# Kernel optimization log

Measured on AMD Instinct MI355X. Metric: run time of the kernel, lower is better.

## Reference

```python
import jax, jax.numpy as jnp
import numpy as np

B, L, D = 8, 2048, 1024

def setup_inputs() -> dict:
    key = jax.random.key(0)
    ks = jax.random.split(key, 12)
    s = 1.0 / np.sqrt(D)
    return {
        "q": jax.random.normal(ks[0], (B, L, D), jnp.float32),
        "k": jax.random.normal(ks[1], (B, L, D), jnp.float32),
        "v": jax.random.normal(ks[2], (B, L, D), jnp.float32),
        "mask": jnp.ones((B, L), jnp.float32),
        # Linear params stored as [in, out] so y = x @ W + b
        "Wq": jax.random.normal(ks[3], (D, D), jnp.float32) * s,
        "bq": jnp.zeros((D,), jnp.float32),
        "Wk": jax.random.normal(ks[4], (D, D), jnp.float32) * s,
        "bk": jnp.zeros((D,), jnp.float32),
        "Wv": jax.random.normal(ks[5], (D, D), jnp.float32) * s,
        "bv": jnp.zeros((D,), jnp.float32),
        "Wg": jax.random.normal(ks[6], (2 * D, D), jnp.float32) * (1.0 / np.sqrt(2 * D)),
        "bg": jnp.zeros((D,), jnp.float32),
    }

def reference(q, k, v, mask, Wq, bq, Wk, bk, Wv, bv, Wg, bg):
    q0 = q
    qp = q @ Wq + bq          # [B, Lq, D]
    kp = k @ Wk + bk          # [B, Lk, D]
    vp = v @ Wv + bv          # [B, Lk, D]
    scale = 1.0 / jnp.sqrt(jnp.asarray(qp.shape[-1], qp.dtype))
    w = jnp.einsum('bqd,bkd->bqk', qp, kp) * scale
    w = jax.nn.softmax(w, axis=-1)          # dim=2 == last axis for 3-D
    x = jnp.einsum('bqk,bkd->bqd', w, vp)
    gate = jnp.concatenate((qp, x), axis=-1) @ Wg + bg
    x = x * mask[..., None]
    x = x * jax.nn.sigmoid(gate)
    return x + q0  # add=True
```

## Files before the change

### kernel.cpp

```cpp
#include <hip/hip_runtime.h>

typedef unsigned int u32;
typedef unsigned short u16;
using v4f    = __attribute__((ext_vector_type(4))) float;
using short8 = __attribute__((ext_vector_type(8))) short;

#define GAS __attribute__((address_space(1)))
#define LAS __attribute__((address_space(3)))

__device__ __forceinline__ u16 f2bf(float f){
  u32 u = __builtin_bit_cast(u32, f);
  u32 r = (u + 0x7fffu + ((u >> 16) & 1u)) >> 16;
  return (u16)r;
}
__device__ __forceinline__ float bf2f(u16 h){
  u32 u = ((u32)h) << 16;
  return __builtin_bit_cast(float, u);
}

__device__ __forceinline__ void gld_lds16(const void* g, void* l){
  __builtin_amdgcn_global_load_lds((const GAS u32*)g, (LAS u32*)l, 16, 0, 0);
}

__global__ __launch_bounds__(256) void cvt_f32_bf16(
    const float* __restrict__ in, u16* __restrict__ out)
{
  const size_t i = ((size_t)blockIdx.x * 256 + threadIdx.x) * 8;
  v4f lo = *(const v4f*)(in + i);
  v4f hi = *(const v4f*)(in + i + 4);
  u32 p0 = (u32)f2bf(lo.x) | ((u32)f2bf(lo.y) << 16);
  u32 p1 = (u32)f2bf(lo.z) | ((u32)f2bf(lo.w) << 16);
  u32 p2 = (u32)f2bf(hi.x) | ((u32)f2bf(hi.y) << 16);
  u32 p3 = (u32)f2bf(hi.z) | ((u32)f2bf(hi.w) << 16);
  *(uint4*)(out + i) = make_uint4(p0, p1, p2, p3);
}

__global__ __launch_bounds__(256) void transpose_w_bf16(
    const float* __restrict__ in, u16* __restrict__ out, int K, int N)
{
  __shared__ float t[64][65];
  const int k0 = blockIdx.x * 64, n0 = blockIdx.y * 64;
  const int tx = threadIdx.x & 63, ty = threadIdx.x >> 6;
  #pragma unroll
  for (int i = 0; i < 16; i++){
    int r = ty + i * 4;
    t[r][tx] = in[(size_t)(k0 + r) * N + (n0 + tx)];
  }
  __syncthreads();
  #pragma unroll
  for (int i = 0; i < 16; i++){
    int r = ty + i * 4;
    out[(size_t)(n0 + r) * K + (k0 + tx)] = f2bf(t[tx][r]);
  }
}

__global__ __launch_bounds__(256) void softmax_rows(u16* __restrict__ S){
  const int lane = threadIdx.x & 63, wid = threadIdx.x >> 6;
  u16* p = S + ((size_t)blockIdx.x * 4 + wid) * 2048;
  uint4 u[4];
  #pragma unroll
  for (int j = 0; j < 4; j++) u[j] = ((const uint4*)p)[lane + j * 64];
  float f[32];
  #pragma unroll
  for (int j = 0; j < 4; j++){
    u32 w4[4] = {u[j].x, u[j].y, u[j].z, u[j].w};
    #pragma unroll
    for (int i = 0; i < 4; i++){
      f[j * 8 + 2*i]     = bf2f((u16)(w4[i] & 0xffffu));
      f[j * 8 + 2*i + 1] = bf2f((u16)(w4[i] >> 16));
    }
  }
  float m = f[0];
  #pragma unroll
  for (int i = 1; i < 32; i++) m = fmaxf(m, f[i]);
  #pragma unroll
  for (int o = 32; o >= 1; o >>= 1) m = fmaxf(m, __shfl_xor(m, o));
  float s = 0.f;
  #pragma unroll
  for (int i = 0; i < 32; i++){ f[i] = __expf(f[i] - m); s += f[i]; }
  #pragma unroll
  for (int o = 32; o >= 1; o >>= 1) s += __shfl_xor(s, o);
  const float inv = 1.f / s;
  #pragma unroll
  for (int j = 0; j < 4; j++){
    u32 w4[4];
    #pragma unroll
    for (int i = 0; i < 4; i++)
      w4[i] = (u32)f2bf(f[j * 8 + 2*i] * inv) |
              ((u32)f2bf(f[j * 8 + 2*i + 1] * inv) << 16);
    ((uint4*)p)[lane + j * 64] = make_uint4(w4[0], w4[1], w4[2], w4[3]);
  }
}

#define MFMA8(B0, B1, N0, N1)                                               \
    __builtin_amdgcn_s_setprio(1);                                          \
    _Pragma("unroll")                                                       \
    for (int mi = 0; mi < 8; mi++){                                         \
      acc[mi][N0] = __builtin_amdgcn_mfma_f32_16x16x32_bf16(                \
                      a[mi], (B0), acc[mi][N0], 0, 0, 0);                   \
      acc[mi][N1] = __builtin_amdgcn_mfma_f32_16x16x32_bf16(                \
                      a[mi], (B1), acc[mi][N1], 0, 0, 0);                   \
    }                                                                       \
    __builtin_amdgcn_s_setprio(0);

template<int AMODE, int EPI>
__global__ __launch_bounds__(512, 2) void gemm256(
    const u16* __restrict__ Ab,
    const u16* __restrict__ A2b,
    const u16* __restrict__ BT,
    int lda, int ldb, int K,
    void* __restrict__ Cout, int ldc,
    const float* __restrict__ bias, float scale,
    size_t aBatch, size_t bBatch, size_t cBatch,
    const u16* __restrict__ xg,
    const float* __restrict__ maskp,
    const float* __restrict__ q0p)
{
  constexpr int BK = 64;
  __shared__ __align__(16) u16 As[2][2][128 * 64];
  __shared__ __align__(16) u16 Bs[2][2][128 * 64];

  const int z   = blockIdx.z;
  const int gx   = (int)gridDim.x;
  const int lin  = (int)blockIdx.y * gx + (int)blockIdx.x;
  const int l2gx = 31 - __clz(gx);
  const int g    = lin >> (3 + l2gx);
  const int rem  = lin & ((gx << 3) - 1);
  const int m0   = ((g << 3) + (rem & 7)) * 256;
  const int n0   = (rem >> 3) * 256;

  const int tid  = (int)threadIdx.x;
  const int lane = tid & 63, wid = tid >> 6;
  const int wm   = (wid >> 2) * 128;
  const int wn   = (wid & 3) * 64;
  const int wnh  = wn >> 7;
  const int wnl  = wn & 127;

  const u16* Az = Ab + (size_t)z * aBatch;
  const u16* Bz = BT + (size_t)z * bBatch;

  u32 offA[2][2], offB[2][2], ldsOffB[2];
  #pragma unroll
  for (int i = 0; i < 2; i++){
    int idx = tid + i * 512;
    int r = idx >> 3, c8 = idx & 7;
    int c8s = c8 ^ (r & 7);
    #pragma unroll
    for (int h = 0; h < 2; h++){
      offA[h][i] = (u32)(((m0 + h * 128 + r) * lda + c8s * 8) * 2);
      offB[h][i] = (u32)(((n0 + h * 128 + r) * ldb + c8s * 8) * 2);
    }
    ldsOffB[i] = (u32)(idx * 16);
  }

  auto stage = [&](int kt, int dbuf){
    const u16* Asrc; u32 ka;
    if (AMODE == 2){
      Asrc = (kt * BK < 1024) ? Az : A2b;
      ka = (u32)(((kt * BK) & 1023) * 2);
    } else {
      Asrc = Az;
      ka = (u32)(kt * BK * 2);
    }
    const u32 kb = (u32)(kt * BK * 2);
    #pragma unroll
    for (int h = 0; h < 2; h++){
      #pragma unroll
      for (int i = 0; i < 2; i++){
        gld_lds16((const char*)Asrc + offA[h][i] + ka,
                  (char*)&As[dbuf][h][0] + ldsOffB[i]);
        gld_lds16((const char*)Bz + offB[h][i] + kb,
                  (char*)&Bs[dbuf][h][0] + ldsOffB[i]);
      }
    }
  };

  v4f acc[8][4];
  #pragma unroll
  for (int mi = 0; mi < 8; mi++)
    #pragma unroll
    for (int ni = 0; ni < 4; ni++)
      acc[mi][ni] = (v4f){0.f, 0.f, 0.f, 0.f};

  const int ll  = lane & 15, lq = lane >> 4;
  const int ch0 = ((0 + lq) ^ (ll & 7)) << 3;
  const int ch4 = ((4 + lq) ^ (ll & 7)) << 3;

  stage(0, 0);
  const int nt = K / BK;
  for (int kt = 0; kt < nt; kt++){
    const int buf = kt & 1;

    asm volatile("s_waitcnt lgkmcnt(0)" ::: "memory");
    __builtin_amdgcn_sched_barrier(0);
    __builtin_amdgcn_s_barrier();
    asm volatile("" ::: "memory");
    if (kt + 1 < nt){
      stage(kt + 1, buf ^ 1);
      asm volatile("s_waitcnt vmcnt(8)" ::: "memory");
    } else {
      asm volatile("s_waitcnt vmcnt(0)" ::: "memory");
    }
    __builtin_amdgcn_s_barrier();
    asm volatile("" ::: "memory");
    __builtin_amdgcn_sched_barrier(0);

    const u16* aB = &As[buf][wid >> 2][0] + ll * 64;
    const u16* bB = &Bs[buf][wnh][0] + (wnl + ll) * 64;

    short8 a[8], b0[2], b1[2], p0[2], p1[2];
    b0[0] = *(const short8*)(bB + ch0);
    b0[1] = *(const short8*)(bB + ch0 + 1024);
    #pragma unroll
    for (int mi = 0; mi < 8; mi++) a[mi] = *(const short8*)(aB + ch0 + mi * 1024);
    b1[0] = *(const short8*)(bB + ch0 + 2048);
    b1[1] = *(const short8*)(bB + ch0 + 3072);
    MFMA8(b0[0], b0[1], 0, 1)
    p0[0] = *(const short8*)(bB + ch4);
    p0[1] = *(const short8*)(bB + ch4 + 1024);
    MFMA8(b1[0], b1[1], 2, 3)
    p1[0] = *(const short8*)(bB + ch4 + 2048);
    p1[1] = *(const short8*)(bB + ch4 + 3072);
    __builtin_amdgcn_sched_barrier(0);
    #pragma unroll
    for (int mi = 0; mi < 8; mi++) a[mi] = *(const short8*)(aB + ch4 + mi * 1024);
    MFMA8(p0[0], p0[1], 0, 1)
    MFMA8(p1[0], p1[1], 2, 3)
  }

  const int lr = lq * 4, lc = ll;
  if (EPI == 0 || EPI == 1){
    u16* C = (u16*)Cout + (size_t)z * cBatch;
    #pragma unroll
    for (int mi = 0; mi < 8; mi++){
      #pragma unroll
      for (int ni = 0; ni < 4; ni++){
        int col = n0 + wn + ni * 16 + lc;
        float bv = (EPI == 0) ? bias[col] : 0.f;
        #pragma unroll
        for (int r = 0; r < 4; r++){
          int row = m0 + wm + mi * 16 + lr + r;
          C[(size_t)row * ldc + col] = f2bf(acc[mi][ni][r] * scale + bv);
        }
      }
    }
  } else if (EPI == 3){
    u16* C = (u16*)Cout;
    #pragma unroll
    for (int mi = 0; mi < 8; mi++){
      int rowb = m0 + wm + mi * 16 + lr;
      int bb   = rowb >> 11;
      int rloc = rowb & 2047;
      #pragma unroll
      for (int ni = 0; ni < 4; ni++){
        int col = n0 + wn + ni * 16 + lc;
        float bv = bias[col];
        u32 pk0 = (u32)f2bf(acc[mi][ni][0] + bv) | ((u32)f2bf(acc[mi][ni][1] + bv) << 16);
        u32 pk1 = (u32)f2bf(acc[mi][ni][2] + bv) | ((u32)f2bf(acc[mi][ni][3] + bv) << 16);
        *(uint2*)&C[(size_t)bb * (1024ull * 2048) + (size_t)col * 2048 + rloc] =
            make_uint2(pk0, pk1);
      }
    }
  } else {
    float* C = (float*)Cout;
    #pragma unroll
    for (int mi = 0; mi < 8; mi++){
      #pragma unroll
      for (int ni = 0; ni < 4; ni++){
        int col = n0 + wn + ni * 16 + lc;
        float bv = bias[col];
        #pragma unroll
        for (int r = 0; r < 4; r++){
          int row = m0 + wm + mi * 16 + lr + r;
          float gg = acc[mi][ni][r] + bv;
          float sg = 1.f / (1.f + __expf(-gg));
          float xv = bf2f(xg[(size_t)row * 1024 + col]);
          C[(size_t)row * ldc + col] =
              xv * maskp[row] * sg + q0p[(size_t)row * 1024 + col];
        }
      }
    }
  }
}
#undef MFMA8

template<int AMODE, int EPI>
__global__ __launch_bounds__(256) void gemm128(
    const float* __restrict__ Af,
    const u16* __restrict__ Ab,
    const u16* __restrict__ A2b,
    const u16* __restrict__ BT,
    int lda, int ldb, int K,
    void* __restrict__ Cout, int ldc,
    const float* __restrict__ bias, float scale,
    size_t aBatch, size_t bBatch, size_t cBatch,
    const u16* __restrict__ xg,
    const float* __restrict__ maskp,
    const float* __restrict__ q0p)
{
  constexpr int BM = 128, BN = 128, BK = 64;
  __shared__ __align__(16) u16 As[BM * BK];
  __shared__ __align__(16) u16 Bs[BN * BK];
  const int z   = blockIdx.z;
  const int lin  = blockIdx.y * gridDim.x + blockIdx.x;
  const int l2gx = 31 - __clz((int)gridDim.x);
  const int g    = lin >> (3 + l2gx);
  const int rem  = lin & (((int)gridDim.x << 3) - 1);
  const int m0   = ((g << 3) + (rem & 7)) * BM;
  const int n0   = (rem >> 3) * BN;
  const int tid = threadIdx.x;
  const int lane = tid & 63, wid = tid >> 6;
  const int wm = (wid >> 1) * 64, wn = (wid & 1) * 64;
  const u16* Abz = Ab + (size_t)z * aBatch;
  const u16* BTz = BT + (size_t)z * bBatch;

  v4f acc[4][4];
  #pragma unroll
  for (int mi = 0; mi < 4; mi++)
    #pragma unroll
    for (int ni = 0; ni < 4; ni++)
      acc[mi][ni] = (v4f){0.f, 0.f, 0.f, 0.f};

  for (int k0 = 0; k0 < K; k0 += BK){
    if (AMODE == 0){
      #pragma unroll
      for (int i = 0; i < 4; i++){
        int idx = tid + i * 256;
        int r = idx >> 3, s = idx & 7;
        const float* src = Af + (size_t)(m0 + r) * lda + (k0 + s * 8);
        v4f lo = ((const v4f*)src)[0];
        v4f hi = ((const v4f*)src)[1];
        u32 p0 = (u32)f2bf(lo.x) | ((u32)f2bf(lo.y) << 16);
        u32 p1 = (u32)f2bf(lo.z) | ((u32)f2bf(lo.w) << 16);
        u32 p2 = (u32)f2bf(hi.x) | ((u32)f2bf(hi.y) << 16);
        u32 p3 = (u32)f2bf(hi.z) | ((u32)f2bf(hi.w) << 16);
        *(uint4*)&As[(size_t)idx * 8] = make_uint4(p0, p1, p2, p3);
      }
    } else {
      #pragma unroll
      for (int i = 0; i < 4; i++){
        int idx = tid + i * 256;
        int r = idx >> 3, s = idx & 7;
        int kk = k0 + s * 8;
        const u16* src;
        if (AMODE == 2){
          src = (kk < 1024) ? (Abz + (size_t)(m0 + r) * 1024 + kk)
                            : (A2b + (size_t)(m0 + r) * 1024 + (kk - 1024));
        } else {
          src = Abz + (size_t)(m0 + r) * lda + kk;
        }
        gld_lds16(src, &As[(size_t)idx * 8]);
      }
    }
    #pragma unroll
    for (int i = 0; i < 4; i++){
      int idx = tid + i * 256;
      int r = idx >> 3, s = idx & 7;
      gld_lds16(BTz + (size_t)(n0 + r) * ldb + (k0 + s * 8), &Bs[(size_t)idx * 8]);
    }
    __syncthreads();
    #pragma unroll
    for (int ks = 0; ks < BK; ks += 32){
      short8 a[4], b[4];
      #pragma unroll
      for (int mi = 0; mi < 4; mi++)
        a[mi] = *(const short8*)&As[(wm + mi * 16 + (lane & 15)) * BK + ks + (lane >> 4) * 8];
      #pragma unroll
      for (int ni = 0; ni < 4; ni++)
        b[ni] = *(const short8*)&Bs[(wn + ni * 16 + (lane & 15)) * BK + ks + (lane >> 4) * 8];
      #pragma unroll
      for (int mi = 0; mi < 4; mi++)
        #pragma unroll
        for (int ni = 0; ni < 4; ni++)
          acc[mi][ni] = __builtin_amdgcn_mfma_f32_16x16x32_bf16(a[mi], b[ni], acc[mi][ni], 0, 0, 0);
    }
    __syncthreads();
  }

  const int lr = (lane >> 4) * 4, lc = lane & 15;
  if (EPI == 0 || EPI == 1){
    u16* C = (u16*)Cout + (size_t)z * cBatch;
    #pragma unroll
    for (int mi = 0; mi < 4; mi++){
      #pragma unroll
      for (int ni = 0; ni < 4; ni++){
        int col = n0 + wn + ni * 16 + lc;
        float bv = (EPI == 0) ? bias[col] : 0.f;
        #pragma unroll
        for (int r = 0; r < 4; r++){
          int row = m0 + wm + mi * 16 + lr + r;
          C[(size_t)row * ldc + col] = f2bf(acc[mi][ni][r] * scale + bv);
        }
      }
    }
  } else if (EPI == 3){
    u16* C = (u16*)Cout;
    #pragma unroll
    for (int mi = 0; mi < 4; mi++){
      int rowb = m0 + wm + mi * 16 + lr;
      int b    = rowb >> 11;
      int rloc = rowb & 2047;
      #pragma unroll
      for (int ni = 0; ni < 4; ni++){
        int col = n0 + wn + ni * 16 + lc;
        float bv = bias[col];
        u32 pk[2];
        pk[0] = (u32)f2bf(acc[mi][ni][0] + bv) | ((u32)f2bf(acc[mi][ni][1] + bv) << 16);
        pk[1] = (u32)f2bf(acc[mi][ni][2] + bv) | ((u32)f2bf(acc[mi][ni][3] + bv) << 16);
        *(uint2*)&C[(size_t)b * (1024ull * 2048) + (size_t)col * 2048 + rloc] =
            make_uint2(pk[0], pk[1]);
      }
    }
  } else {
    float* C = (float*)Cout;
    #pragma unroll
    for (int mi = 0; mi < 4; mi++){
      #pragma unroll
      for (int ni = 0; ni < 4; ni++){
        int col = n0 + wn + ni * 16 + lc;
        float bv = bias[col];
        #pragma unroll
        for (int r = 0; r < 4; r++){
          int row = m0 + wm + mi * 16 + lr + r;
          float g  = acc[mi][ni][r] + bv;
          float sg = 1.f / (1.f + __expf(-g));
          float xv = bf2f(xg[(size_t)row * 1024 + col]);
          C[(size_t)row * ldc + col] =
              xv * maskp[row] * sg + q0p[(size_t)row * 1024 + col];
        }
      }
    }
  }
}

extern "C" void kernel_launch(void* const* d_in, const int* in_sizes, int n_in,
                              void* d_out, int out_size, void* d_ws, size_t ws_size,
                              hipStream_t stream)
{
  const float* q    = (const float*)d_in[0];
  const float* k    = (const float*)d_in[1];
  const float* v    = (const float*)d_in[2];
  const float* mask = (const float*)d_in[3];
  const float* Wq   = (const float*)d_in[4];
  const float* bq   = (const float*)d_in[5];
  const float* Wk   = (const float*)d_in[6];
  const float* bk   = (const float*)d_in[7];
  const float* Wv   = (const float*)d_in[8];
  const float* bv   = (const float*)d_in[9];
  const float* Wg   = (const float*)d_in[10];
  const float* bg   = (const float*)d_in[11];
  float* out = (float*)d_out;

  char* ws = (char*)d_ws;
  const size_t MB = 1024ull * 1024ull;
  u16* WqT = (u16*)(ws + 0 * MB);
  u16* WkT = (u16*)(ws + 2 * MB);
  u16* WvT = (u16*)(ws + 4 * MB);
  u16* WgT = (u16*)(ws + 6 * MB);
  u16* qp  = (u16*)(ws + 10 * MB);
  u16* kp  = (u16*)(ws + 42 * MB);
  u16* vpT = (u16*)(ws + 74 * MB);
  u16* S   = (u16*)(ws + 106 * MB);
  u16* tmp = (u16*)(ws + 106 * MB);
  u16* x   = kp;

  const bool bigws = ws_size >= 138 * MB;
  int nb = 8;
  while (nb > 1 && 106 * MB + (size_t)nb * 8 * MB > ws_size) nb >>= 1;
  const int nchunks = 8 / nb;

  dim3 B(256);
  dim3 T5(512);

  transpose_w_bf16<<<dim3(16, 16, 1), B, 0, stream>>>(Wq, WqT, 1024, 1024);
  transpose_w_bf16<<<dim3(16, 16, 1), B, 0, stream>>>(Wk, WkT, 1024, 1024);
  transpose_w_bf16<<<dim3(16, 16, 1), B, 0, stream>>>(Wv, WvT, 1024, 1024);
  transpose_w_bf16<<<dim3(32, 16, 1), B, 0, stream>>>(Wg, WgT, 2048, 1024);

  if (bigws){
    cvt_f32_bf16<<<dim3(8192), B, 0, stream>>>(q, tmp);
    gemm256<1, 0><<<dim3(4, 64, 1), T5, 0, stream>>>(tmp, nullptr, WqT,
        1024, 1024, 1024, qp, 1024, bq, 1.f, 0, 0, 0, nullptr, nullptr, nullptr);
    cvt_f32_bf16<<<dim3(8192), B, 0, stream>>>(k, tmp);
    gemm256<1, 0><<<dim3(4, 64, 1), T5, 0, stream>>>(tmp, nullptr, WkT,
        1024, 1024, 1024, kp, 1024, bk, 1.f, 0, 0, 0, nullptr, nullptr, nullptr);
    cvt_f32_bf16<<<dim3(8192), B, 0, stream>>>(v, tmp);
    gemm256<1, 3><<<dim3(4, 64, 1), T5, 0, stream>>>(tmp, nullptr, WvT,
        1024, 1024, 1024, vpT, 0, bv, 1.f, 0, 0, 0, nullptr, nullptr, nullptr);

    for (int c = 0; c < nchunks; c++){
      const size_t boff = (size_t)c * nb;
      gemm256<1, 1><<<dim3(8, 8, nb), T5, 0, stream>>>(
          qp + boff * 2048 * 1024, nullptr, kp + boff * 2048 * 1024,
          1024, 1024, 1024, S, 2048, nullptr, 0.03125f,
          2048ull * 1024, 2048ull * 1024, 2048ull * 2048, nullptr, nullptr, nullptr);
      softmax_rows<<<dim3(nb * 512, 1, 1), B, 0, stream>>>(S);
      gemm256<1, 1><<<dim3(4, 8, nb), T5, 0, stream>>>(
          S, nullptr, vpT + boff * 1024 * 2048,
          2048, 2048, 2048, x + boff * 2048 * 1024, 1024, nullptr, 1.f,
          2048ull * 2048, 1024ull * 2048, 2048ull * 1024, nullptr, nullptr, nullptr);
    }

    gemm256<2, 2><<<dim3(4, 64, 1), T5, 0, stream>>>(qp, x, WgT,
        1024, 2048, 2048, out, 1024, bg, 1.f, 0, 0, 0, x, mask, q);
  } else {
    gemm128<0, 0><<<dim3(8, 128, 1), B, 0, stream>>>(q, nullptr, nullptr, WqT,
        1024, 1024, 1024, qp, 1024, bq, 1.f, 0, 0, 0, nullptr, nullptr, nullptr);
    gemm128<0, 0><<<dim3(8, 128, 1), B, 0, stream>>>(k, nullptr, nullptr, WkT,
        1024, 1024, 1024, kp, 1024, bk, 1.f, 0, 0, 0, nullptr, nullptr, nullptr);
    gemm128<0, 3><<<dim3(8, 128, 1), B, 0, stream>>>(v, nullptr, nullptr, WvT,
        1024, 1024, 1024, vpT, 0, bv, 1.f, 0, 0, 0, nullptr, nullptr, nullptr);

    for (int c = 0; c < nchunks; c++){
      const size_t boff = (size_t)c * nb;
      gemm128<1, 1><<<dim3(16, 16, nb), B, 0, stream>>>(nullptr,
          qp + boff * 2048 * 1024, nullptr, kp + boff * 2048 * 1024,
          1024, 1024, 1024, S, 2048, nullptr, 0.03125f,
          2048ull * 1024, 2048ull * 1024, 2048ull * 2048, nullptr, nullptr, nullptr);
      softmax_rows<<<dim3(nb * 512, 1, 1), B, 0, stream>>>(S);
      gemm128<1, 1><<<dim3(8, 16, nb), B, 0, stream>>>(nullptr,
          S, nullptr, vpT + boff * 1024 * 2048,
          2048, 2048, 2048, x + boff * 2048 * 1024, 1024, nullptr, 1.f,
          2048ull * 2048, 1024ull * 2048, 2048ull * 1024, nullptr, nullptr, nullptr);
    }

    gemm128<2, 2><<<dim3(8, 128, 1), B, 0, stream>>>(nullptr, qp, x, WgT,
        1024, 2048, 2048, out, 1024, bg, 1.f, 0, 0, 0, x, mask, q);
  }
}
```

Baseline: 643.0 us.

## Fuse fp32-to-bf16 conversion into projection GEMM and interleave prefetch with MFMA phases

Removes the three standalone cvt_f32_bf16 kernels and has the projection GEMMs read fp32 activations directly into registers, convert them to bf16 and write them to LDS. The main loop is also restructured so next-tile global-to-LDS loads are issued in four quarters between MFMA groups, with barriers around each group, replacing the single prefetch block and the split b/p registers. The aim is to save the extra round trip through HBM for the converted inputs and to overlap loads with compute. The cost is more barriers per k-step, a full vmcnt(0) wait at the top of each iteration, and more register pressure now that the occupancy hint of 2 in launch_bounds is dropped, which also affects the attention GEMMs.

```diff
diff --git a/kernel.cpp b/kernel.cpp
--- a/kernel.cpp
+++ b/kernel.cpp
@@ -20,19 +20,6 @@
 
 __device__ __forceinline__ void gld_lds16(const void* g, void* l){
   __builtin_amdgcn_global_load_lds((const GAS u32*)g, (LAS u32*)l, 16, 0, 0);
-}
-
-__global__ __launch_bounds__(256) void cvt_f32_bf16(
-    const float* __restrict__ in, u16* __restrict__ out)
-{
-  const size_t i = ((size_t)blockIdx.x * 256 + threadIdx.x) * 8;
-  v4f lo = *(const v4f*)(in + i);
-  v4f hi = *(const v4f*)(in + i + 4);
-  u32 p0 = (u32)f2bf(lo.x) | ((u32)f2bf(lo.y) << 16);
-  u32 p1 = (u32)f2bf(lo.z) | ((u32)f2bf(lo.w) << 16);
-  u32 p2 = (u32)f2bf(hi.x) | ((u32)f2bf(hi.y) << 16);
-  u32 p3 = (u32)f2bf(hi.z) | ((u32)f2bf(hi.w) << 16);
-  *(uint4*)(out + i) = make_uint4(p0, p1, p2, p3);
 }
 
 __global__ __launch_bounds__(256) void transpose_w_bf16(
@@ -91,6 +78,10 @@
     ((uint4*)p)[lane + j * 64] = make_uint4(w4[0], w4[1], w4[2], w4[3]);
   }
 }
+
+#define BAR() do{ asm volatile("" ::: "memory");                            \
+                  __builtin_amdgcn_s_barrier();                             \
+                  asm volatile("" ::: "memory"); }while(0)
 
 #define MFMA8(B0, B1, N0, N1)                                               \
     __builtin_amdgcn_s_setprio(1);                                          \
@@ -104,7 +95,8 @@
     __builtin_amdgcn_s_setprio(0);
 
 template<int AMODE, int EPI>
-__global__ __launch_bounds__(512, 2) void gemm256(
+__global__ __launch_bounds__(512) void gemm256(
+    const float* __restrict__ Af,
     const u16* __restrict__ Ab,
     const u16* __restrict__ A2b,
     const u16* __restrict__ BT,
@@ -139,7 +131,7 @@
   const u16* Az = Ab + (size_t)z * aBatch;
   const u16* Bz = BT + (size_t)z * bBatch;
 
-  u32 offA[2][2], offB[2][2], ldsOffB[2];
+  u32 offA[2][2], offB[2][2], ldsOff[2];
   #pragma unroll
   for (int i = 0; i < 2; i++){
     int idx = tid + i * 512;
@@ -150,29 +142,55 @@
       offA[h][i] = (u32)(((m0 + h * 128 + r) * lda + c8s * 8) * 2);
       offB[h][i] = (u32)(((n0 + h * 128 + r) * ldb + c8s * 8) * 2);
     }
-    ldsOffB[i] = (u32)(idx * 16);
-  }
-
-  auto stage = [&](int kt, int dbuf){
-    const u16* Asrc; u32 ka;
-    if (AMODE == 2){
-      Asrc = (kt * BK < 1024) ? Az : A2b;
-      ka = (u32)(((kt * BK) & 1023) * 2);
-    } else {
-      Asrc = Az;
-      ka = (u32)(kt * BK * 2);
-    }
+    ldsOff[i] = (u32)(idx * 16);
+  }
+
+  auto stageQ = [&](int kt, int dbuf, int q){
+    const int h = q >> 1, i = q & 1;
     const u32 kb = (u32)(kt * BK * 2);
-    #pragma unroll
-    for (int h = 0; h < 2; h++){
+    if (AMODE != 0){
+      const u16* Asrc; u32 ka;
+      if (AMODE == 2){
+        Asrc = (kt * BK < 1024) ? Az : A2b;
+        ka = (u32)(((kt * BK) & 1023) * 2);
+      } else {
+        Asrc = Az;
+        ka = (u32)(kt * BK * 2);
+      }
+      gld_lds16((const char*)Asrc + offA[h][i] + ka,
+                (char*)&As[dbuf][h][0] + ldsOff[i]);
+    }
+    gld_lds16((const char*)Bz + offB[h][i] + kb,
+              (char*)&Bs[dbuf][h][0] + ldsOff[i]);
+  };
+
+  v4f afr[2][2][2];
+  auto loadA = [&](int kt){
+    if (AMODE != 0) return;
+    #pragma unroll
+    for (int h = 0; h < 2; h++)
       #pragma unroll
       for (int i = 0; i < 2; i++){
-        gld_lds16((const char*)Asrc + offA[h][i] + ka,
-                  (char*)&As[dbuf][h][0] + ldsOffB[i]);
-        gld_lds16((const char*)Bz + offB[h][i] + kb,
-                  (char*)&Bs[dbuf][h][0] + ldsOffB[i]);
-      }
-    }
+        int idx = tid + i * 512;
+        int r = idx >> 3, c8s = (idx & 7) ^ (r & 7);
+        const float* src = Af + (size_t)(m0 + h * 128 + r) * lda + kt * BK + c8s * 8;
+        afr[h][i][0] = ((const v4f*)src)[0];
+        afr[h][i][1] = ((const v4f*)src)[1];
+      }
+  };
+  auto writeA = [&](int dbuf){
+    if (AMODE != 0) return;
+    #pragma unroll
+    for (int h = 0; h < 2; h++)
+      #pragma unroll
+      for (int i = 0; i < 2; i++){
+        int idx = tid + i * 512;
+        u32 q0 = (u32)f2bf(afr[h][i][0].x) | ((u32)f2bf(afr[h][i][0].y) << 16);
+        u32 q1 = (u32)f2bf(afr[h][i][0].z) | ((u32)f2bf(afr[h][i][0].w) << 16);
+        u32 q2 = (u32)f2bf(afr[h][i][1].x) | ((u32)f2bf(afr[h][i][1].y) << 16);
+        u32 q3 = (u32)f2bf(afr[h][i][1].z) | ((u32)f2bf(afr[h][i][1].w) << 16);
+        *(uint4*)((char*)&As[dbuf][h][0] + idx * 16) = make_uint4(q0, q1, q2, q3);
+      }
   };
 
   v4f acc[8][4];
@@ -186,46 +204,61 @@
   const int ch0 = ((0 + lq) ^ (ll & 7)) << 3;
   const int ch4 = ((4 + lq) ^ (ll & 7)) << 3;
 
-  stage(0, 0);
+  if (AMODE == 0){
+    loadA(0);
+    #pragma unroll
+    for (int q = 0; q < 4; q++) stageQ(0, 0, q);
+    writeA(0);
+  } else {
+    #pragma unroll
+    for (int q = 0; q < 4; q++) stageQ(0, 0, q);
+  }
+
   const int nt = K / BK;
   for (int kt = 0; kt < nt; kt++){
     const int buf = kt & 1;
-
-    asm volatile("s_waitcnt lgkmcnt(0)" ::: "memory");
-    __builtin_amdgcn_sched_barrier(0);
-    __builtin_amdgcn_s_barrier();
-    asm volatile("" ::: "memory");
-    if (kt + 1 < nt){
-      stage(kt + 1, buf ^ 1);
-      asm volatile("s_waitcnt vmcnt(8)" ::: "memory");
-    } else {
-      asm volatile("s_waitcnt vmcnt(0)" ::: "memory");
-    }
-    __builtin_amdgcn_s_barrier();
-    asm volatile("" ::: "memory");
-    __builtin_amdgcn_sched_barrier(0);
+    const bool pf = (kt + 1 < nt);
+
+    asm volatile("s_waitcnt vmcnt(0)" ::: "memory");
+    if (AMODE == 0) asm volatile("s_waitcnt lgkmcnt(0)" ::: "memory");
+    BAR();
+
+    if (pf) loadA(kt + 1);
 
     const u16* aB = &As[buf][wid >> 2][0] + ll * 64;
     const u16* bB = &Bs[buf][wnh][0] + (wnl + ll) * 64;
 
-    short8 a[8], b0[2], b1[2], p0[2], p1[2];
-    b0[0] = *(const short8*)(bB + ch0);
-    b0[1] = *(const short8*)(bB + ch0 + 1024);
+    short8 a[8], b[2];
+    b[0] = *(const short8*)(bB + ch0);
+    b[1] = *(const short8*)(bB + ch0 + 1024);
     #pragma unroll
     for (int mi = 0; mi < 8; mi++) a[mi] = *(const short8*)(aB + ch0 + mi * 1024);
-    b1[0] = *(const short8*)(bB + ch0 + 2048);
-    b1[1] = *(const short8*)(bB + ch0 + 3072);
-    MFMA8(b0[0], b0[1], 0, 1)
-    p0[0] = *(const short8*)(bB + ch4);
-    p0[1] = *(const short8*)(bB + ch4 + 1024);
-    MFMA8(b1[0], b1[1], 2, 3)
-    p1[0] = *(const short8*)(bB + ch4 + 2048);
-    p1[1] = *(const short8*)(bB + ch4 + 3072);
-    __builtin_amdgcn_sched_barrier(0);
+    if (pf) stageQ(kt + 1, buf ^ 1, 0);
+    BAR();
+    MFMA8(b[0], b[1], 0, 1)
+    BAR();
+    b[0] = *(const short8*)(bB + ch0 + 2048);
+    b[1] = *(const short8*)(bB + ch0 + 3072);
+    if (pf) stageQ(kt + 1, buf ^ 1, 1);
+    BAR();
+    MFMA8(b[0], b[1], 2, 3)
+    BAR();
+    b[0] = *(const short8*)(bB + ch4);
+    b[1] = *(const short8*)(bB + ch4 + 1024);
     #pragma unroll
     for (int mi = 0; mi < 8; mi++) a[mi] = *(const short8*)(aB + ch4 + mi * 1024);
-    MFMA8(p0[0], p0[1], 0, 1)
-    MFMA8(p1[0], p1[1], 2, 3)
+    if (pf) stageQ(kt + 1, buf ^ 1, 2);
+    BAR();
+    MFMA8(b[0], b[1], 0, 1)
+    BAR();
+    b[0] = *(const short8*)(bB + ch4 + 2048);
+    b[1] = *(const short8*)(bB + ch4 + 3072);
+    if (pf) stageQ(kt + 1, buf ^ 1, 3);
+    BAR();
+    MFMA8(b[0], b[1], 2, 3)
+    BAR();
+
+    if (pf) writeA(buf ^ 1);
   }
 
   const int lr = lq * 4, lc = ll;
@@ -283,6 +316,7 @@
   }
 }
 #undef MFMA8
+#undef BAR
 
 template<int AMODE, int EPI>
 __global__ __launch_bounds__(256) void gemm128(
@@ -461,7 +495,6 @@
   u16* kp  = (u16*)(ws + 42 * MB);
   u16* vpT = (u16*)(ws + 74 * MB);
   u16* S   = (u16*)(ws + 106 * MB);
-  u16* tmp = (u16*)(ws + 106 * MB);
   u16* x   = kp;
 
   const bool bigws = ws_size >= 138 * MB;
@@ -478,30 +511,27 @@
   transpose_w_bf16<<<dim3(32, 16, 1), B, 0, stream>>>(Wg, WgT, 2048, 1024);
 
   if (bigws){
-    cvt_f32_bf16<<<dim3(8192), B, 0, stream>>>(q, tmp);
-    gemm256<1, 0><<<dim3(4, 64, 1), T5, 0, stream>>>(tmp, nullptr, WqT,
+    gemm256<0, 0><<<dim3(4, 64, 1), T5, 0, stream>>>(q, nullptr, nullptr, WqT,
         1024, 1024, 1024, qp, 1024, bq, 1.f, 0, 0, 0, nullptr, nullptr, nullptr);
-    cvt_f32_bf16<<<dim3(8192), B, 0, stream>>>(k, tmp);
-    gemm256<1, 0><<<dim3(4, 64, 1), T5, 0, stream>>>(tmp, nullptr, WkT,
+    gemm256<0, 0><<<dim3(4, 64, 1), T5, 0, stream>>>(k, nullptr, nullptr, WkT,
         1024, 1024, 1024, kp, 1024, bk, 1.f, 0, 0, 0, nullptr, nullptr, nullptr);
-    cvt_f32_bf16<<<dim3(8192), B, 0, stream>>>(v, tmp);
-    gemm256<1, 3><<<dim3(4, 64, 1), T5, 0, stream>>>(tmp, nullptr, WvT,
+    gemm256<0, 3><<<dim3(4, 64, 1), T5, 0, stream>>>(v, nullptr, nullptr, WvT,
         1024, 1024, 1024, vpT, 0, bv, 1.f, 0, 0, 0, nullptr, nullptr, nullptr);
 
     for (int c = 0; c < nchunks; c++){
       const size_t boff = (size_t)c * nb;
-      gemm256<1, 1><<<dim3(8, 8, nb), T5, 0, stream>>>(
+      gemm256<1, 1><<<dim3(8, 8, nb), T5, 0, stream>>>(nullptr,
           qp + boff * 2048 * 1024, nullptr, kp + boff * 2048 * 1024,
           1024, 1024, 1024, S, 2048, nullptr, 0.03125f,
           2048ull * 1024, 2048ull * 1024, 2048ull * 2048, nullptr, nullptr, nullptr);
       softmax_rows<<<dim3(nb * 512, 1, 1), B, 0, stream>>>(S);
-      gemm256<1, 1><<<dim3(4, 8, nb), T5, 0, stream>>>(
+      gemm256<1, 1><<<dim3(4, 8, nb), T5, 0, stream>>>(nullptr,
           S, nullptr, vpT + boff * 1024 * 2048,
           2048, 2048, 2048, x + boff * 2048 * 1024, 1024, nullptr, 1.f,
           2048ull * 2048, 1024ull * 2048, 2048ull * 1024, nullptr, nullptr, nullptr);
     }
 
-    gemm256<2, 2><<<dim3(4, 64, 1), T5, 0, stream>>>(qp, x, WgT,
+    gemm256<2, 2><<<dim3(4, 64, 1), T5, 0, stream>>>(nullptr, qp, x, WgT,
         1024, 2048, 2048, out, 1024, bg, 1.f, 0, 0, 0, x, mask, q);
   } else {
     gemm128<0, 0><<<dim3(8, 128, 1), B, 0, stream>>>(q, nullptr, nullptr, WqT,
```

Measured after the change: 662.4 us. 3.0% more time.

## Replace 256x256 GEMM main loop with 8-phase interleaved load/MFMA pipeline

Applied to the files above, without the earlier changes.

Rewrites the bf16 GEMM main loop as an eight-phase schedule over two K-tiles per iteration. Each phase reads a quarter of the LDS fragments, issues part of the next tiles' global-to-LDS loads, and runs a 16-MFMA burst at raised priority between barriers. The LDS layout changes to flat 256-row tiles with a new row mapping for the B loads. The aim is to hide global-load and LDS-read latency behind matrix math at finer granularity, in the style of ping-pong pipelines. The cost is many more barriers per K-step and dropping the min-blocks-per-SM launch bound, which may reduce occupancy. The loop also assumes the K-tile count is even.

```diff
diff --git a/kernel.cpp b/kernel.cpp
--- a/kernel.cpp
+++ b/kernel.cpp
@@ -92,19 +92,41 @@
   }
 }
 
-#define MFMA8(B0, B1, N0, N1)                                               \
-    __builtin_amdgcn_s_setprio(1);                                          \
-    _Pragma("unroll")                                                       \
-    for (int mi = 0; mi < 8; mi++){                                         \
-      acc[mi][N0] = __builtin_amdgcn_mfma_f32_16x16x32_bf16(                \
-                      a[mi], (B0), acc[mi][N0], 0, 0, 0);                   \
-      acc[mi][N1] = __builtin_amdgcn_mfma_f32_16x16x32_bf16(                \
-                      a[mi], (B1), acc[mi][N1], 0, 0, 0);                   \
-    }                                                                       \
-    __builtin_amdgcn_s_setprio(0);
+#define RD_A(BUFP, RH)                                                       \
+  do{ _Pragma("unroll") for (int f = 0; f < 4; f++){                         \
+    af[f][0] = *(const short8*)((BUFP) + ((RH)*4+f)*1024 + ch0);             \
+    af[f][1] = *(const short8*)((BUFP) + ((RH)*4+f)*1024 + ch4); } }while(0)
+
+#define RD_B(BUFP, BX, C)                                                    \
+  do{ _Pragma("unroll") for (int cf = 0; cf < 2; cf++){                      \
+    BX[cf][0] = *(const short8*)((BUFP) + ((C)*2+cf)*1024 + ch0);            \
+    BX[cf][1] = *(const short8*)((BUFP) + ((C)*2+cf)*1024 + ch4); } }while(0)
+
+#define MM16(RH, C, BX)                                                      \
+  do{ _Pragma("unroll") for (int f = 0; f < 4; f++){                         \
+    acc[(RH)*4+f][(C)*2]   = __builtin_amdgcn_mfma_f32_16x16x32_bf16(        \
+        af[f][0], BX[0][0], acc[(RH)*4+f][(C)*2],   0, 0, 0);                \
+    acc[(RH)*4+f][(C)*2]   = __builtin_amdgcn_mfma_f32_16x16x32_bf16(        \
+        af[f][1], BX[0][1], acc[(RH)*4+f][(C)*2],   0, 0, 0);                \
+    acc[(RH)*4+f][(C)*2+1] = __builtin_amdgcn_mfma_f32_16x16x32_bf16(        \
+        af[f][0], BX[1][0], acc[(RH)*4+f][(C)*2+1], 0, 0, 0);                \
+    acc[(RH)*4+f][(C)*2+1] = __builtin_amdgcn_mfma_f32_16x16x32_bf16(        \
+        af[f][1], BX[1][1], acc[(RH)*4+f][(C)*2+1], 0, 0, 0); } }while(0)
+
+#define PH_OPEN()                                                            \
+  __builtin_amdgcn_s_barrier();                                              \
+  asm volatile("s_waitcnt lgkmcnt(0)" ::: "memory");                         \
+  __builtin_amdgcn_sched_barrier(0);                                         \
+  __builtin_amdgcn_s_setprio(1)
+
+#define PH_CLOSE()                                                           \
+  __builtin_amdgcn_s_setprio(0);                                             \
+  asm volatile("" ::: "memory");                                             \
+  __builtin_amdgcn_s_barrier();                                              \
+  asm volatile("" ::: "memory")
 
 template<int AMODE, int EPI>
-__global__ __launch_bounds__(512, 2) void gemm256(
+__global__ __launch_bounds__(512) void gemm8p(
     const u16* __restrict__ Ab,
     const u16* __restrict__ A2b,
     const u16* __restrict__ BT,
@@ -117,10 +139,10 @@
     const float* __restrict__ q0p)
 {
   constexpr int BK = 64;
-  __shared__ __align__(16) u16 As[2][2][128 * 64];
-  __shared__ __align__(16) u16 Bs[2][2][128 * 64];
-
-  const int z   = blockIdx.z;
+  __shared__ __align__(16) u16 As[2][256 * 64];
+  __shared__ __align__(16) u16 Bs[2][256 * 64];
+
+  const int z    = blockIdx.z;
   const int gx   = (int)gridDim.x;
   const int lin  = (int)blockIdx.y * gx + (int)blockIdx.x;
   const int l2gx = 31 - __clz(gx);
@@ -133,46 +155,44 @@
   const int lane = tid & 63, wid = tid >> 6;
   const int wm   = (wid >> 2) * 128;
   const int wn   = (wid & 3) * 64;
-  const int wnh  = wn >> 7;
-  const int wnl  = wn & 127;
 
   const u16* Az = Ab + (size_t)z * aBatch;
   const u16* Bz = BT + (size_t)z * bBatch;
 
-  u32 offA[2][2], offB[2][2], ldsOffB[2];
-  #pragma unroll
-  for (int i = 0; i < 2; i++){
-    int idx = tid + i * 512;
-    int r = idx >> 3, c8 = idx & 7;
-    int c8s = c8 ^ (r & 7);
-    #pragma unroll
-    for (int h = 0; h < 2; h++){
-      offA[h][i] = (u32)(((m0 + h * 128 + r) * lda + c8s * 8) * 2);
-      offB[h][i] = (u32)(((n0 + h * 128 + r) * ldb + c8s * 8) * 2);
-    }
-    ldsOffB[i] = (u32)(idx * 16);
-  }
-
-  auto stage = [&](int kt, int dbuf){
-    const u16* Asrc; u32 ka;
+  const int qrow = tid >> 3, c8 = tid & 7;
+  u32 aG[2][2], aL[2][2], bG[2][2], bL[2][2];
+  #pragma unroll
+  for (int u = 0; u < 2; u++)
+    #pragma unroll
+    for (int j = 0; j < 2; j++){
+      int ra = qrow + u * 64 + j * 128;
+      int ca = c8 ^ (ra & 7);
+      aG[u][j] = (u32)(((m0 + ra) * lda + ca * 8) * 2);
+      aL[u][j] = (u32)(ra * 128 + c8 * 16);
+      int rb = (qrow & 31) + (qrow >> 5) * 64 + u * 32 + j * 128;
+      int cb = c8 ^ (rb & 7);
+      bG[u][j] = (u32)(((n0 + rb) * ldb + cb * 8) * 2);
+      bL[u][j] = (u32)(rb * 128 + c8 * 16);
+    }
+
+  auto stA = [&](int kt, int bf, int u){
+    const u16* src; u32 ka;
     if (AMODE == 2){
-      Asrc = (kt * BK < 1024) ? Az : A2b;
+      src = (kt * BK < 1024) ? Az : A2b;
       ka = (u32)(((kt * BK) & 1023) * 2);
     } else {
-      Asrc = Az;
+      src = Az;
       ka = (u32)(kt * BK * 2);
     }
+    #pragma unroll
+    for (int j = 0; j < 2; j++)
+      gld_lds16((const char*)src + aG[u][j] + ka, (char*)&As[bf][0] + aL[u][j]);
+  };
+  auto stB = [&](int kt, int bf, int u){
     const u32 kb = (u32)(kt * BK * 2);
     #pragma unroll
-    for (int h = 0; h < 2; h++){
-      #pragma unroll
-      for (int i = 0; i < 2; i++){
-        gld_lds16((const char*)Asrc + offA[h][i] + ka,
-                  (char*)&As[dbuf][h][0] + ldsOffB[i]);
-        gld_lds16((const char*)Bz + offB[h][i] + kb,
-                  (char*)&Bs[dbuf][h][0] + ldsOffB[i]);
-      }
-    }
+    for (int j = 0; j < 2; j++)
+      gld_lds16((const char*)Bz + bG[u][j] + kb, (char*)&Bs[bf][0] + bL[u][j]);
   };
 
   v4f acc[8][4];
@@ -186,46 +206,61 @@
   const int ch0 = ((0 + lq) ^ (ll & 7)) << 3;
   const int ch4 = ((4 + lq) ^ (ll & 7)) << 3;
 
-  stage(0, 0);
+  const u16* aP0 = &As[0][0] + (wm + ll) * 64;
+  const u16* bP0 = &Bs[0][0] + (wn + ll) * 64;
+  const u16* aP1 = &As[1][0] + (wm + ll) * 64;
+  const u16* bP1 = &Bs[1][0] + (wn + ll) * 64;
+
+  stA(0, 0, 0); stA(0, 0, 1); stB(0, 0, 0); stB(0, 0, 1);
+  stA(1, 1, 0); stB(1, 1, 0); stB(1, 1, 1);
+  asm volatile("s_waitcnt vmcnt(6)" ::: "memory");
+  __builtin_amdgcn_s_barrier();
+  asm volatile("" ::: "memory");
+
   const int nt = K / BK;
-  for (int kt = 0; kt < nt; kt++){
-    const int buf = kt & 1;
-
-    asm volatile("s_waitcnt lgkmcnt(0)" ::: "memory");
-    __builtin_amdgcn_sched_barrier(0);
+  const int nIter = nt >> 1;
+  short8 af[4][2], bf0[2][2], bf1[2][2];
+
+  for (int it = 0; it < nIter; it++){
+    const int t0 = 2 * it, t1 = t0 + 1;
+    const bool s2 = (t0 + 2 < nt);
+    const bool s3 = (t0 + 3 < nt);
+    const bool lastIt = (it == nIter - 1);
+
+    RD_A(aP0, 0); RD_B(bP0, bf0, 0);
+    stA(t1, 1, 1);
+    PH_OPEN(); MM16(0, 0, bf0); PH_CLOSE();
+    RD_B(bP0, bf1, 1);
+    if (s2) stA(t0 + 2, 0, 0);
+    PH_OPEN(); MM16(0, 1, bf1); PH_CLOSE();
+    RD_A(aP0, 1);
+    if (s2) stB(t0 + 2, 0, 0);
+    PH_OPEN(); MM16(1, 0, bf0); PH_CLOSE();
+    if (s2) stB(t0 + 2, 0, 1);
+    PH_OPEN(); MM16(1, 1, bf1);
+    __builtin_amdgcn_s_setprio(0);
+    if (lastIt) asm volatile("s_waitcnt vmcnt(0)" ::: "memory");
+    else        asm volatile("s_waitcnt vmcnt(6)" ::: "memory");
+    asm volatile("" ::: "memory");
     __builtin_amdgcn_s_barrier();
     asm volatile("" ::: "memory");
-    if (kt + 1 < nt){
-      stage(kt + 1, buf ^ 1);
-      asm volatile("s_waitcnt vmcnt(8)" ::: "memory");
-    } else {
-      asm volatile("s_waitcnt vmcnt(0)" ::: "memory");
-    }
+
+    RD_A(aP1, 0); RD_B(bP1, bf0, 0);
+    if (s2) stA(t0 + 2, 0, 1);
+    PH_OPEN(); MM16(0, 0, bf0); PH_CLOSE();
+    RD_B(bP1, bf1, 1);
+    if (s3) stA(t0 + 3, 1, 0);
+    PH_OPEN(); MM16(0, 1, bf1); PH_CLOSE();
+    RD_A(aP1, 1);
+    if (s3) stB(t0 + 3, 1, 0);
+    PH_OPEN(); MM16(1, 0, bf0); PH_CLOSE();
+    if (s3) stB(t0 + 3, 1, 1);
+    PH_OPEN(); MM16(1, 1, bf1);
+    __builtin_amdgcn_s_setprio(0);
+    asm volatile("s_waitcnt vmcnt(6)" ::: "memory");
+    asm volatile("" ::: "memory");
     __builtin_amdgcn_s_barrier();
     asm volatile("" ::: "memory");
-    __builtin_amdgcn_sched_barrier(0);
-
-    const u16* aB = &As[buf][wid >> 2][0] + ll * 64;
-    const u16* bB = &Bs[buf][wnh][0] + (wnl + ll) * 64;
-
-    short8 a[8], b0[2], b1[2], p0[2], p1[2];
-    b0[0] = *(const short8*)(bB + ch0);
-    b0[1] = *(const short8*)(bB + ch0 + 1024);
-    #pragma unroll
-    for (int mi = 0; mi < 8; mi++) a[mi] = *(const short8*)(aB + ch0 + mi * 1024);
-    b1[0] = *(const short8*)(bB + ch0 + 2048);
-    b1[1] = *(const short8*)(bB + ch0 + 3072);
-    MFMA8(b0[0], b0[1], 0, 1)
-    p0[0] = *(const short8*)(bB + ch4);
-    p0[1] = *(const short8*)(bB + ch4 + 1024);
-    MFMA8(b1[0], b1[1], 2, 3)
-    p1[0] = *(const short8*)(bB + ch4 + 2048);
-    p1[1] = *(const short8*)(bB + ch4 + 3072);
-    __builtin_amdgcn_sched_barrier(0);
-    #pragma unroll
-    for (int mi = 0; mi < 8; mi++) a[mi] = *(const short8*)(aB + ch4 + mi * 1024);
-    MFMA8(p0[0], p0[1], 0, 1)
-    MFMA8(p1[0], p1[1], 2, 3)
   }
 
   const int lr = lq * 4, lc = ll;
@@ -282,7 +317,11 @@
     }
   }
 }
-#undef MFMA8
+#undef RD_A
+#undef RD_B
+#undef MM16
+#undef PH_OPEN
+#undef PH_CLOSE
 
 template<int AMODE, int EPI>
 __global__ __launch_bounds__(256) void gemm128(
@@ -479,29 +518,29 @@
 
   if (bigws){
     cvt_f32_bf16<<<dim3(8192), B, 0, stream>>>(q, tmp);
-    gemm256<1, 0><<<dim3(4, 64, 1), T5, 0, stream>>>(tmp, nullptr, WqT,
+    gemm8p<1, 0><<<dim3(4, 64, 1), T5, 0, stream>>>(tmp, nullptr, WqT,
         1024, 1024, 1024, qp, 1024, bq, 1.f, 0, 0, 0, nullptr, nullptr, nullptr);
     cvt_f32_bf16<<<dim3(8192), B, 0, stream>>>(k, tmp);
-    gemm256<1, 0><<<dim3(4, 64, 1), T5, 0, stream>>>(tmp, nullptr, WkT,
+    gemm8p<1, 0><<<dim3(4, 64, 1), T5, 0, stream>>>(tmp, nullptr, WkT,
         1024, 1024, 1024, kp, 1024, bk, 1.f, 0, 0, 0, nullptr, nullptr, nullptr);
     cvt_f32_bf16<<<dim3(8192), B, 0, stream>>>(v, tmp);
-    gemm256<1, 3><<<dim3(4, 64, 1), T5, 0, stream>>>(tmp, nullptr, WvT,
+    gemm8p<1, 3><<<dim3(4, 64, 1), T5, 0, stream>>>(tmp, nullptr, WvT,
         1024, 1024, 1024, vpT, 0, bv, 1.f, 0, 0, 0, nullptr, nullptr, nullptr);
 
     for (int c = 0; c < nchunks; c++){
       const size_t boff = (size_t)c * nb;
-      gemm256<1, 1><<<dim3(8, 8, nb), T5, 0, stream>>>(
+      gemm8p<1, 1><<<dim3(8, 8, nb), T5, 0, stream>>>(
           qp + boff * 2048 * 1024, nullptr, kp + boff * 2048 * 1024,
           1024, 1024, 1024, S, 2048, nullptr, 0.03125f,
           2048ull * 1024, 2048ull * 1024, 2048ull * 2048, nullptr, nullptr, nullptr);
       softmax_rows<<<dim3(nb * 512, 1, 1), B, 0, stream>>>(S);
-      gemm256<1, 1><<<dim3(4, 8, nb), T5, 0, stream>>>(
+      gemm8p<1, 1><<<dim3(4, 8, nb), T5, 0, stream>>>(
           S, nullptr, vpT + boff * 1024 * 2048,
           2048, 2048, 2048, x + boff * 2048 * 1024, 1024, nullptr, 1.f,
           2048ull * 2048, 1024ull * 2048, 2048ull * 1024, nullptr, nullptr, nullptr);
     }
 
-    gemm256<2, 2><<<dim3(4, 64, 1), T5, 0, stream>>>(qp, x, WgT,
+    gemm8p<2, 2><<<dim3(4, 64, 1), T5, 0, stream>>>(qp, x, WgT,
         1024, 2048, 2048, out, 1024, bg, 1.f, 0, 0, 0, x, mask, q);
   } else {
     gemm128<0, 0><<<dim3(8, 128, 1), B, 0, stream>>>(q, nullptr, nullptr, WqT,
```

New measurement: 586.0 us. -8.9%, faster.
